# Kernel optimization log

Measured on AMD Instinct MI355X. Metric: run time of the kernel, lower is better.

## Reference

```python
import jax, jax.numpy as jnp
import numpy as np
from jax import lax

DUNITS = 1024
ATT_DIM = 512
EPROJS = 512
ACONV_CHANS = 10
ACONV_FILTS = 100  # kernel size = 2*100+1 = 201
H_LEN = 16384
N_PREV = 128
SCALING = 2.0


def setup_inputs() -> dict:
    key = jax.random.key(0)
    ks = jax.random.split(key, 10)
    inv = lambda fan_in: 1.0 / np.sqrt(fan_in)
    return {
        "dec_z": jax.random.normal(ks[0], (1, DUNITS), jnp.float32),
        "att_prev": jax.random.uniform(ks[1], (N_PREV, 1, H_LEN), jnp.float32) / H_LEN,
        "pre_compute_enc_h": jax.random.normal(ks[2], (1, H_LEN, ATT_DIM), jnp.float32),
        "enc_h": jax.random.normal(ks[3], (1, H_LEN, EPROJS), jnp.float32),
        "mask": jnp.zeros((1, H_LEN), jnp.float32),
        # parameters (torch default inits, scale by 1/sqrt(fan_in))
        "loc_conv_w": jax.random.normal(ks[4], (ACONV_CHANS, 1, 2 * ACONV_FILTS + 1), jnp.float32) * inv(2 * ACONV_FILTS + 1),
        "mlp_att_w": jax.random.normal(ks[5], (ATT_DIM, ACONV_CHANS), jnp.float32) * inv(ACONV_CHANS),
        "mlp_dec_w": jax.random.normal(ks[6], (ATT_DIM, DUNITS), jnp.float32) * inv(DUNITS),
        "gvec_w": jax.random.normal(ks[7], (1, ATT_DIM), jnp.float32) * inv(ATT_DIM),
        "gvec_b": jnp.zeros((1,), jnp.float32),
    }


def reference(dec_z, att_prev, pre_compute_enc_h, enc_h, mask,
              loc_conv_w, mlp_att_w, mlp_dec_w, gvec_w, gvec_b):
    h_length = enc_h.shape[1]
    dec_z = dec_z.reshape(1, DUNITS)

    # coverage vector: sum of all previous attention distributions -> [1, h]
    cov_vec = jnp.sum(att_prev, axis=0)

    # location conv: Conv2d(1, C, (1, 2F+1)) on [1,1,1,h] == 1D conv on [1,1,h]
    att_conv = lax.conv_general_dilated(
        cov_vec[:, None, :], loc_conv_w,
        window_strides=(1,), padding=[(ACONV_FILTS, ACONV_FILTS)],
        dimension_numbers=("NCH", "OIH", "NCH"),
    )  # [1, C, h]
    # squeeze/transpose then mlp_att (no bias): [1, h, att_dim]
    att_conv = jnp.einsum("bch,ac->bha", att_conv, mlp_att_w)

    # mlp_dec (no bias), tiled over h: [1, 1, att_dim]
    dec_z_tiled = (dec_z @ mlp_dec_w.T)[:, None, :]

    # additive attention score e: [1, h]
    t = jnp.tanh(att_conv + pre_compute_enc_h + dec_z_tiled)
    e = jnp.einsum("bha,oa->bho", t, gvec_w)[..., 0] + gvec_b
    e = e + mask

    w = jax.nn.softmax(SCALING * e, axis=1)  # [1, h]

    att_prev_new = jnp.concatenate([att_prev, w[None]], axis=0)  # [n+1, 1, h]
    c = jnp.sum(enc_h * w[:, :, None], axis=1)  # [1, eprojs]
    return (c, att_prev_new)
```

## Files before the change

### kernel.cpp

```cpp
#include <hip/hip_runtime.h>

#define H_LEN 16384
#define ATT_DIM 512
#define DUNITS 1024
#define EPROJS 512
#define NCH 10
#define KFILT 201
#define PAD 100
#define N_PREV 128
#define NB_SCORE 512
#define NB_FIN 256
#define NCOVP 16

__global__ __launch_bounds__(256) void k_prep(const float* __restrict__ att_prev,
                                              const float* __restrict__ mlp_dec_w,
                                              const float* __restrict__ dec_z,
                                              float* __restrict__ out_prev,
                                              float* __restrict__ cov16,
                                              float* __restrict__ dz,
                                              float* __restrict__ out_c) {
    int b = blockIdx.x, tid = threadIdx.x;
    if (b < 256) {
        const float4* ap4 = (const float4*)att_prev;
        float4* op4 = (float4*)out_prev;
        float4* cv4 = (float4*)cov16;
        int hb = b >> 4, q = b & 15;
        int idx0 = hb * 256 + tid;
        float4 s = {0.f, 0.f, 0.f, 0.f};
        #pragma unroll
        for (int n = q * 8; n < q * 8 + 8; ++n) {
            float4 v = ap4[n * (H_LEN / 4) + idx0];
            s.x += v.x; s.y += v.y; s.z += v.z; s.w += v.w;
            op4[n * (H_LEN / 4) + idx0] = v;
        }
        cv4[q * (H_LEN / 4) + idx0] = s;
    } else if (b < 384) {
        int lane = tid & 63;
        int a = (b - 256) * 4 + (tid >> 6);
        const float* row = mlp_dec_w + a * DUNITS;
        float s = 0.f;
        #pragma unroll
        for (int t = 0; t < DUNITS / 64; ++t) s += row[lane + 64 * t] * dec_z[lane + 64 * t];
        #pragma unroll
        for (int off = 32; off > 0; off >>= 1) s += __shfl_xor(s, off, 64);
        if (lane == 0) dz[a] = s;
    } else {
        out_c[tid] = 0.f;
        out_c[tid + 256] = 0.f;
    }
}

__global__ __launch_bounds__(256, 2) void k_score(const float* __restrict__ cov16,
                                                  const float* __restrict__ cw,
                                                  const float* __restrict__ pre,
                                                  const float* __restrict__ mask,
                                                  const float* __restrict__ dz,
                                                  const float* __restrict__ watt,
                                                  const float* __restrict__ gv,
                                                  const float* __restrict__ gb,
                                                  const float* __restrict__ enc,
                                                  float* __restrict__ vbuf,
                                                  float* __restrict__ pm,
                                                  float* __restrict__ ps,
                                                  float* __restrict__ pcb) {
    __shared__ float cov_s[32 + 2 * PAD];
    __shared__ float mask_s[32];
    __shared__ float pc[8][NCH][32];
    __shared__ float cf[NCH][32];
    __shared__ float vt[32];
    __shared__ float wt[32];

    int tid = threadIdx.x, b = blockIdx.x;
    int h0 = b * 32;
    int lane = tid & 63, wv = tid >> 6;
    int a0 = lane * 4;

    for (int i = tid; i < 32 + 2 * PAD; i += 256) {
        int g = h0 - PAD + i;
        float s = 0.f;
        if (g >= 0 && g < H_LEN) {
            #pragma unroll
            for (int q = 0; q < NCOVP; ++q) s += cov16[q * H_LEN + g];
        }
        cov_s[i] = s;
    }
    if (tid < 32) mask_s[tid] = mask[h0 + tid];

    const float4* pre4 = (const float4*)pre;
    int hbase = h0 + wv * 8;
    float4 P[16];
    #pragma unroll
    for (int j = 0; j < 8; ++j) {
        P[2 * j]     = pre4[(hbase + j) * 128 + lane];
        P[2 * j + 1] = pre4[(hbase + j) * 128 + 64 + lane];
    }

    float Wr[8][NCH], dzr[8], gvr[8];
    #pragma unroll
    for (int i = 0; i < 8; ++i) {
        int a = (i < 4) ? (a0 + i) : (a0 + 256 + (i - 4));
        dzr[i] = dz[a];
        gvr[i] = gv[a];
        #pragma unroll
        for (int c = 0; c < NCH; ++c) Wr[i][c] = watt[a * NCH + c];
    }
    float bias = gb[0];
    __syncthreads();

    {
        int h = tid & 31, q = tid >> 5;
        int k0 = (q * KFILT) / 8, k1 = ((q + 1) * KFILT) / 8;
        float acc[NCH];
        #pragma unroll
        for (int c = 0; c < NCH; ++c) acc[c] = 0.f;
        for (int k = k0; k < k1; ++k) {
            float s = cov_s[h + k];
            #pragma unroll
            for (int c = 0; c < NCH; ++c) acc[c] += s * cw[c * KFILT + k];
        }
        #pragma unroll
        for (int c = 0; c < NCH; ++c) pc[q][c][h] = acc[c];
    }
    __syncthreads();
    for (int i = tid; i < NCH * 32; i += 256) {
        int c = i >> 5, h = i & 31;
        float s = 0.f;
        #pragma unroll
        for (int q = 0; q < 8; ++q) s += pc[q][c][h];
        cf[c][h] = s;
    }
    __syncthreads();

    #pragma unroll
    for (int j = 0; j < 8; ++j) {
        int hh = wv * 8 + j;
        float ch[NCH];
        #pragma unroll
        for (int c = 0; c < NCH; ++c) ch[c] = cf[c][hh];
        float4 c0 = P[2 * j], c1 = P[2 * j + 1];
        float pv[8] = {c0.x, c0.y, c0.z, c0.w, c1.x, c1.y, c1.z, c1.w};
        float eacc = 0.f;
        #pragma unroll
        for (int i = 0; i < 8; ++i) {
            float x = pv[i] + dzr[i];
            #pragma unroll
            for (int c = 0; c < NCH; ++c) x += ch[c] * Wr[i][c];
            x = fminf(fmaxf(x, -15.f), 15.f);
            float z = __expf(2.f * x);
            float t = (z - 1.f) * __builtin_amdgcn_rcpf(z + 1.f);
            eacc += t * gvr[i];
        }
        #pragma unroll
        for (int off = 32; off > 0; off >>= 1) eacc += __shfl_xor(eacc, off, 64);
        if (lane == 0) {
            float v = 2.f * (eacc + bias + mask_s[hh]);
            vt[hh] = v;
            vbuf[h0 + hh] = v;
        }
    }
    __syncthreads();

    if (wv == 0) {
        float v = (lane < 32) ? vt[lane] : -1e30f;
        float m = v;
        #pragma unroll
        for (int off = 32; off > 0; off >>= 1) m = fmaxf(m, __shfl_xor(m, off, 64));
        float ev = (lane < 32) ? __expf(v - m) : 0.f;
        if (lane < 32) wt[lane] = ev;
        float s = ev;
        #pragma unroll
        for (int off = 32; off > 0; off >>= 1) s += __shfl_xor(s, off, 64);
        if (lane == 0) { pm[b] = m; ps[b] = s; }
    }
    __syncthreads();

    const float2* enc2 = (const float2*)enc;
    float2 acc0 = {0.f, 0.f}, acc1 = {0.f, 0.f};
    #pragma unroll
    for (int h = 0; h < 32; h += 2) {
        float w0 = wt[h], w1 = wt[h + 1];
        float2 e0 = enc2[(h0 + h) * 256 + tid];
        float2 e1 = enc2[(h0 + h + 1) * 256 + tid];
        acc0.x += w0 * e0.x; acc0.y += w0 * e0.y;
        acc1.x += w1 * e1.x; acc1.y += w1 * e1.y;
    }
    float2 acc = {acc0.x + acc1.x, acc0.y + acc1.y};
    ((float2*)pcb)[b * 256 + tid] = acc;
}

__global__ __launch_bounds__(256) void k_final(const float* __restrict__ vbuf,
                                               const float* __restrict__ pm,
                                               const float* __restrict__ ps,
                                               const float* __restrict__ pcb,
                                               float* __restrict__ out_w,
                                               float* __restrict__ out_c) {
    __shared__ float redA[4], redB[4];
    int tid = threadIdx.x, b = blockIdx.x;
    int lane = tid & 63, wv = tid >> 6;

    float m0 = pm[tid], m1 = pm[tid + 256];
    float s0 = ps[tid], s1 = ps[tid + 256];
    float m = fmaxf(m0, m1);
    #pragma unroll
    for (int off = 32; off > 0; off >>= 1) m = fmaxf(m, __shfl_xor(m, off, 64));
    if (lane == 0) redA[wv] = m;
    __syncthreads();
    float M = fmaxf(fmaxf(redA[0], redA[1]), fmaxf(redA[2], redA[3]));
    float s = s0 * __expf(m0 - M) + s1 * __expf(m1 - M);
    #pragma unroll
    for (int off = 32; off > 0; off >>= 1) s += __shfl_xor(s, off, 64);
    if (lane == 0) redB[wv] = s;
    __syncthreads();
    float S = redB[0] + redB[1] + redB[2] + redB[3];
    float rinv = 1.f / S;

    if (tid < 64) {
        int h = b * 64 + tid;
        out_w[h] = __expf(vbuf[h] - M) * rinv;
    }

    int r0 = 2 * b, r1 = 2 * b + 1;
    float sc0 = __expf(pm[r0] - M) * rinv;
    float sc1 = __expf(pm[r1] - M) * rinv;
    float v0 = pcb[r0 * EPROJS + tid] * sc0 + pcb[r1 * EPROJS + tid] * sc1;
    float v1 = pcb[r0 * EPROJS + tid + 256] * sc0 + pcb[r1 * EPROJS + tid + 256] * sc1;
    atomicAdd(&out_c[tid], v0);
    atomicAdd(&out_c[tid + 256], v1);
}

extern "C" void kernel_launch(void* const* d_in, const int* in_sizes, int n_in,
                              void* d_out, int out_size, void* d_ws, size_t ws_size,
                              hipStream_t stream) {
    const float* dec_z      = (const float*)d_in[0];
    const float* att_prev   = (const float*)d_in[1];
    const float* pre        = (const float*)d_in[2];
    const float* enc_h      = (const float*)d_in[3];
    const float* mask       = (const float*)d_in[4];
    const float* loc_conv_w = (const float*)d_in[5];
    const float* mlp_att_w  = (const float*)d_in[6];
    const float* mlp_dec_w  = (const float*)d_in[7];
    const float* gvec_w     = (const float*)d_in[8];
    const float* gvec_b     = (const float*)d_in[9];

    float* out_c    = (float*)d_out;
    float* out_prev = out_c + EPROJS;
    float* out_w    = out_prev + N_PREV * H_LEN;

    float* ws    = (float*)d_ws;
    float* cov16 = ws;
    float* dz    = cov16 + NCOVP * H_LEN;
    float* vb    = dz + ATT_DIM;
    float* pm    = vb + H_LEN;
    float* ps    = pm + NB_SCORE;
    float* pcb   = ps + NB_SCORE;

    k_prep<<<385, 256, 0, stream>>>(att_prev, mlp_dec_w, dec_z, out_prev, cov16, dz, out_c);
    k_score<<<NB_SCORE, 256, 0, stream>>>(cov16, loc_conv_w, pre, mask, dz, mlp_att_w,
                                          gvec_w, gvec_b, enc_h, vb, pm, ps, pcb);
    k_final<<<NB_FIN, 256, 0, stream>>>(vb, pm, ps, pcb, out_w, out_c);
}
```

Measured before the change: 146.3 us.

## Fuse softmax finalize into score kernel via last-block atomic counter

Removes the separate k_final launch. Each score block now bumps an atomic counter after writing its partials, and the last block to finish computes the global softmax normalisation, writes all attention weights and reduces the 512 context partials without atomics. The warp shuffle reductions for the 8 rows per wave are also batched so they interleave. This saves a kernel launch and the out_c atomics, but it serialises the final reduction of 16K weights and 256K partials onto a single block.

Measured after the change: 219.9 us. 50.4% more time.

```diff
diff --git a/kernel.cpp b/kernel.cpp
--- a/kernel.cpp
+++ b/kernel.cpp
@@ -8,8 +8,7 @@
 #define KFILT 201
 #define PAD 100
 #define N_PREV 128
-#define NB_SCORE 512
-#define NB_FIN 256
+#define NBLK 512
 #define NCOVP 16
 
 __global__ __launch_bounds__(256) void k_prep(const float* __restrict__ att_prev,
@@ -18,7 +17,7 @@
                                               float* __restrict__ out_prev,
                                               float* __restrict__ cov16,
                                               float* __restrict__ dz,
-                                              float* __restrict__ out_c) {
+                                              int* __restrict__ cnt) {
     int b = blockIdx.x, tid = threadIdx.x;
     if (b < 256) {
         const float4* ap4 = (const float4*)att_prev;
@@ -45,8 +44,7 @@
         for (int off = 32; off > 0; off >>= 1) s += __shfl_xor(s, off, 64);
         if (lane == 0) dz[a] = s;
     } else {
-        out_c[tid] = 0.f;
-        out_c[tid + 256] = 0.f;
+        if (tid == 0) *cnt = 0;
     }
 }
 
@@ -62,13 +60,20 @@
                                                   float* __restrict__ vbuf,
                                                   float* __restrict__ pm,
                                                   float* __restrict__ ps,
-                                                  float* __restrict__ pcb) {
+                                                  float* __restrict__ pcb,
+                                                  float* __restrict__ out_w,
+                                                  float* __restrict__ out_c,
+                                                  int* __restrict__ cnt) {
     __shared__ float cov_s[32 + 2 * PAD];
     __shared__ float mask_s[32];
     __shared__ float pc[8][NCH][32];
     __shared__ float cf[NCH][32];
     __shared__ float vt[32];
     __shared__ float wt[32];
+    __shared__ float scale_s[NBLK];
+    __shared__ float4 ctmp[128];
+    __shared__ float redA[4], redB[4];
+    __shared__ int isLast;
 
     int tid = threadIdx.x, b = blockIdx.x;
     int h0 = b * 32;
@@ -131,6 +136,7 @@
     }
     __syncthreads();
 
+    float ea[8];
     #pragma unroll
     for (int j = 0; j < 8; ++j) {
         int hh = wv * 8 + j;
@@ -150,10 +156,18 @@
             float t = (z - 1.f) * __builtin_amdgcn_rcpf(z + 1.f);
             eacc += t * gvr[i];
         }
-        #pragma unroll
-        for (int off = 32; off > 0; off >>= 1) eacc += __shfl_xor(eacc, off, 64);
-        if (lane == 0) {
-            float v = 2.f * (eacc + bias + mask_s[hh]);
+        ea[j] = eacc;
+    }
+    #pragma unroll
+    for (int off = 32; off > 0; off >>= 1) {
+        #pragma unroll
+        for (int j = 0; j < 8; ++j) ea[j] += __shfl_xor(ea[j], off, 64);
+    }
+    if (lane == 0) {
+        #pragma unroll
+        for (int j = 0; j < 8; ++j) {
+            int hh = wv * 8 + j;
+            float v = 2.f * (ea[j] + bias + mask_s[hh]);
             vt[hh] = v;
             vbuf[h0 + hh] = v;
         }
@@ -184,19 +198,15 @@
         acc0.x += w0 * e0.x; acc0.y += w0 * e0.y;
         acc1.x += w1 * e1.x; acc1.y += w1 * e1.y;
     }
-    float2 acc = {acc0.x + acc1.x, acc0.y + acc1.y};
-    ((float2*)pcb)[b * 256 + tid] = acc;
-}
-
-__global__ __launch_bounds__(256) void k_final(const float* __restrict__ vbuf,
-                                               const float* __restrict__ pm,
-                                               const float* __restrict__ ps,
-                                               const float* __restrict__ pcb,
-                                               float* __restrict__ out_w,
-                                               float* __restrict__ out_c) {
-    __shared__ float redA[4], redB[4];
-    int tid = threadIdx.x, b = blockIdx.x;
-    int lane = tid & 63, wv = tid >> 6;
+    float2 accv = {acc0.x + acc1.x, acc0.y + acc1.y};
+    ((float2*)pcb)[b * 256 + tid] = accv;
+
+    __threadfence();
+    __syncthreads();
+    if (tid == 0) isLast = (atomicAdd(cnt, 1) == NBLK - 1);
+    __syncthreads();
+    if (!isLast) return;
+    __threadfence();
 
     float m0 = pm[tid], m1 = pm[tid + 256];
     float s0 = ps[tid], s1 = ps[tid + 256];
@@ -206,26 +216,49 @@
     if (lane == 0) redA[wv] = m;
     __syncthreads();
     float M = fmaxf(fmaxf(redA[0], redA[1]), fmaxf(redA[2], redA[3]));
-    float s = s0 * __expf(m0 - M) + s1 * __expf(m1 - M);
+    float e0 = __expf(m0 - M), e1 = __expf(m1 - M);
+    float s = s0 * e0 + s1 * e1;
     #pragma unroll
     for (int off = 32; off > 0; off >>= 1) s += __shfl_xor(s, off, 64);
     if (lane == 0) redB[wv] = s;
     __syncthreads();
     float S = redB[0] + redB[1] + redB[2] + redB[3];
     float rinv = 1.f / S;
-
-    if (tid < 64) {
-        int h = b * 64 + tid;
-        out_w[h] = __expf(vbuf[h] - M) * rinv;
-    }
-
-    int r0 = 2 * b, r1 = 2 * b + 1;
-    float sc0 = __expf(pm[r0] - M) * rinv;
-    float sc1 = __expf(pm[r1] - M) * rinv;
-    float v0 = pcb[r0 * EPROJS + tid] * sc0 + pcb[r1 * EPROJS + tid] * sc1;
-    float v1 = pcb[r0 * EPROJS + tid + 256] * sc0 + pcb[r1 * EPROJS + tid + 256] * sc1;
-    atomicAdd(&out_c[tid], v0);
-    atomicAdd(&out_c[tid + 256], v1);
+    scale_s[tid] = e0 * rinv;
+    scale_s[tid + 256] = e1 * rinv;
+    __syncthreads();
+
+    {
+        const float4* vb4 = (const float4*)vbuf;
+        float4* ow4 = (float4*)out_w;
+        for (int i = tid; i < H_LEN / 4; i += 256) {
+            float4 v = vb4[i];
+            float4 o = { __expf(v.x - M) * rinv, __expf(v.y - M) * rinv,
+                         __expf(v.z - M) * rinv, __expf(v.w - M) * rinv };
+            ow4[i] = o;
+        }
+    }
+
+    {
+        const float4* pcb4 = (const float4*)pcb;
+        int c = tid & 127, half = tid >> 7;
+        float4 acc = {0.f, 0.f, 0.f, 0.f};
+        int r0 = half * 256;
+        #pragma unroll 4
+        for (int r = r0; r < r0 + 256; ++r) {
+            float sc = scale_s[r];
+            float4 p = pcb4[r * 128 + c];
+            acc.x += sc * p.x; acc.y += sc * p.y;
+            acc.z += sc * p.z; acc.w += sc * p.w;
+        }
+        if (half) ctmp[c] = acc;
+        __syncthreads();
+        if (!half) {
+            float4 o = ctmp[c];
+            acc.x += o.x; acc.y += o.y; acc.z += o.z; acc.w += o.w;
+            ((float4*)out_c)[c] = acc;
+        }
+    }
 }
 
 extern "C" void kernel_launch(void* const* d_in, const int* in_sizes, int n_in,
@@ -251,11 +284,12 @@
     float* dz    = cov16 + NCOVP * H_LEN;
     float* vb    = dz + ATT_DIM;
     float* pm    = vb + H_LEN;
-    float* ps    = pm + NB_SCORE;
-    float* pcb   = ps + NB_SCORE;
-
-    k_prep<<<385, 256, 0, stream>>>(att_prev, mlp_dec_w, dec_z, out_prev, cov16, dz, out_c);
-    k_score<<<NB_SCORE, 256, 0, stream>>>(cov16, loc_conv_w, pre, mask, dz, mlp_att_w,
-                                          gvec_w, gvec_b, enc_h, vb, pm, ps, pcb);
-    k_final<<<NB_FIN, 256, 0, stream>>>(vb, pm, ps, pcb, out_w, out_c);
+    float* ps    = pm + NBLK;
+    float* pcb   = ps + NBLK;
+    int*   cnt   = (int*)(pcb + NBLK * EPROJS);
+
+    k_prep<<<385, 256, 0, stream>>>(att_prev, mlp_dec_w, dec_z, out_prev, cov16, dz, cnt);
+    k_score<<<NBLK, 256, 0, stream>>>(cov16, loc_conv_w, pre, mask, dz, mlp_att_w,
+                                      gvec_w, gvec_b, enc_h, vb, pm, ps, pcb,
+                                      out_w, out_c, cnt);
 }
```

## Remap score work to column-pairs per thread with transposed-reduction across rows

Applied to the files above, without the earlier changes.

Each thread now owns two attention columns for all 32 rows instead of eight columns for eight rows. The pre-computed encoder rows are streamed in float2 chunks, and the mlp_att weights are pre-transposed in k_prep so they load as float2 per channel. Per-row dot products are combined with a butterfly transpose-reduce across lanes followed by a small shared-memory sum over waves, which replaces the eight full wave reductions per wave. This is meant to cut register pressure from the 16 float4 prefetch and the shuffle cost, at the price of holding 32 accumulators per thread and an extra workspace buffer.

Result: faster. 139.2 us (-4.8%).

```diff
diff --git a/kernel.cpp b/kernel.cpp
--- a/kernel.cpp
+++ b/kernel.cpp
@@ -8,6 +8,7 @@
 #define KFILT 201
 #define PAD 100
 #define N_PREV 128
+#define HB 32
 #define NB_SCORE 512
 #define NB_FIN 256
 #define NCOVP 16
@@ -15,9 +16,11 @@
 __global__ __launch_bounds__(256) void k_prep(const float* __restrict__ att_prev,
                                               const float* __restrict__ mlp_dec_w,
                                               const float* __restrict__ dec_z,
+                                              const float* __restrict__ watt,
                                               float* __restrict__ out_prev,
                                               float* __restrict__ cov16,
                                               float* __restrict__ dz,
+                                              float* __restrict__ wattT,
                                               float* __restrict__ out_c) {
     int b = blockIdx.x, tid = threadIdx.x;
     if (b < 256) {
@@ -47,6 +50,12 @@
     } else {
         out_c[tid] = 0.f;
         out_c[tid + 256] = 0.f;
+        int a = tid * 2;
+        #pragma unroll
+        for (int c = 0; c < NCH; ++c) {
+            wattT[c * ATT_DIM + a]     = watt[a * NCH + c];
+            wattT[c * ATT_DIM + a + 1] = watt[(a + 1) * NCH + c];
+        }
     }
 }
 
@@ -55,7 +64,7 @@
                                                   const float* __restrict__ pre,
                                                   const float* __restrict__ mask,
                                                   const float* __restrict__ dz,
-                                                  const float* __restrict__ watt,
+                                                  const float* __restrict__ wattT,
                                                   const float* __restrict__ gv,
                                                   const float* __restrict__ gb,
                                                   const float* __restrict__ enc,
@@ -63,19 +72,18 @@
                                                   float* __restrict__ pm,
                                                   float* __restrict__ ps,
                                                   float* __restrict__ pcb) {
-    __shared__ float cov_s[32 + 2 * PAD];
-    __shared__ float mask_s[32];
-    __shared__ float pc[8][NCH][32];
-    __shared__ float cf[NCH][32];
-    __shared__ float vt[32];
-    __shared__ float wt[32];
+    __shared__ float cov_s[HB + 2 * PAD];
+    __shared__ float mask_s[HB];
+    __shared__ float pc[8][NCH][HB];
+    __shared__ float cfT[HB * 12];
+    __shared__ float ew[4][HB];
+    __shared__ float wt[HB];
 
     int tid = threadIdx.x, b = blockIdx.x;
-    int h0 = b * 32;
+    int h0 = b * HB;
     int lane = tid & 63, wv = tid >> 6;
-    int a0 = lane * 4;
-
-    for (int i = tid; i < 32 + 2 * PAD; i += 256) {
+
+    for (int i = tid; i < HB + 2 * PAD; i += 256) {
         int g = h0 - PAD + i;
         float s = 0.f;
         if (g >= 0 && g < H_LEN) {
@@ -84,25 +92,16 @@
         }
         cov_s[i] = s;
     }
-    if (tid < 32) mask_s[tid] = mask[h0 + tid];
-
-    const float4* pre4 = (const float4*)pre;
-    int hbase = h0 + wv * 8;
-    float4 P[16];
-    #pragma unroll
-    for (int j = 0; j < 8; ++j) {
-        P[2 * j]     = pre4[(hbase + j) * 128 + lane];
-        P[2 * j + 1] = pre4[(hbase + j) * 128 + 64 + lane];
-    }
-
-    float Wr[8][NCH], dzr[8], gvr[8];
-    #pragma unroll
-    for (int i = 0; i < 8; ++i) {
-        int a = (i < 4) ? (a0 + i) : (a0 + 256 + (i - 4));
-        dzr[i] = dz[a];
-        gvr[i] = gv[a];
-        #pragma unroll
-        for (int c = 0; c < NCH; ++c) Wr[i][c] = watt[a * NCH + c];
+    if (tid < HB) mask_s[tid] = mask[h0 + tid];
+
+    int a = (wv << 7) + (lane << 1);
+    float2 dz2 = *(const float2*)(dz + a);
+    float2 gv2 = *(const float2*)(gv + a);
+    float W0[NCH], W1[NCH];
+    #pragma unroll
+    for (int c = 0; c < NCH; ++c) {
+        float2 w = *(const float2*)(wattT + c * ATT_DIM + a);
+        W0[c] = w.x; W1[c] = w.y;
     }
     float bias = gb[0];
     __syncthreads();
@@ -122,51 +121,87 @@
         for (int c = 0; c < NCH; ++c) pc[q][c][h] = acc[c];
     }
     __syncthreads();
-    for (int i = tid; i < NCH * 32; i += 256) {
+    for (int i = tid; i < NCH * HB; i += 256) {
         int c = i >> 5, h = i & 31;
         float s = 0.f;
         #pragma unroll
         for (int q = 0; q < 8; ++q) s += pc[q][c][h];
-        cf[c][h] = s;
-    }
-    __syncthreads();
-
-    #pragma unroll
-    for (int j = 0; j < 8; ++j) {
-        int hh = wv * 8 + j;
-        float ch[NCH];
-        #pragma unroll
-        for (int c = 0; c < NCH; ++c) ch[c] = cf[c][hh];
-        float4 c0 = P[2 * j], c1 = P[2 * j + 1];
-        float pv[8] = {c0.x, c0.y, c0.z, c0.w, c1.x, c1.y, c1.z, c1.w};
-        float eacc = 0.f;
-        #pragma unroll
-        for (int i = 0; i < 8; ++i) {
-            float x = pv[i] + dzr[i];
+        cfT[h * 12 + c] = s;
+    }
+    __syncthreads();
+
+    float ea[HB];
+    const float2* pre2 = (const float2*)pre;
+    int colf2 = (wv << 6) + lane;
+    #pragma unroll
+    for (int hc = 0; hc < HB; hc += 8) {
+        float2 Pr[8];
+        #pragma unroll
+        for (int j = 0; j < 8; ++j) Pr[j] = pre2[(h0 + hc + j) * 256 + colf2];
+        #pragma unroll
+        for (int j = 0; j < 8; ++j) {
+            int h = hc + j;
+            const float4* cp = (const float4*)&cfT[h * 12];
+            float4 c0 = cp[0], c1 = cp[1], c2 = cp[2];
+            float ch[NCH] = {c0.x, c0.y, c0.z, c0.w, c1.x, c1.y, c1.z, c1.w, c2.x, c2.y};
+            float x0 = Pr[j].x + dz2.x;
+            float x1 = Pr[j].y + dz2.y;
             #pragma unroll
-            for (int c = 0; c < NCH; ++c) x += ch[c] * Wr[i][c];
-            x = fminf(fmaxf(x, -15.f), 15.f);
-            float z = __expf(2.f * x);
-            float t = (z - 1.f) * __builtin_amdgcn_rcpf(z + 1.f);
-            eacc += t * gvr[i];
-        }
-        #pragma unroll
-        for (int off = 32; off > 0; off >>= 1) eacc += __shfl_xor(eacc, off, 64);
-        if (lane == 0) {
-            float v = 2.f * (eacc + bias + mask_s[hh]);
-            vt[hh] = v;
-            vbuf[h0 + hh] = v;
-        }
-    }
+            for (int c = 0; c < NCH; ++c) { x0 += ch[c] * W0[c]; x1 += ch[c] * W1[c]; }
+            x0 = fminf(fmaxf(x0, -15.f), 15.f);
+            x1 = fminf(fmaxf(x1, -15.f), 15.f);
+            float z0 = __expf(2.f * x0), z1 = __expf(2.f * x1);
+            float t0 = (z0 - 1.f) * __builtin_amdgcn_rcpf(z0 + 1.f);
+            float t1 = (z1 - 1.f) * __builtin_amdgcn_rcpf(z1 + 1.f);
+            ea[h] = t0 * gv2.x + t1 * gv2.y;
+        }
+    }
+
+    #pragma unroll
+    for (int k = 0; k < 16; ++k) {
+        float up = __shfl_xor(ea[k + 16], 32, 64);
+        float dn = __shfl_xor(ea[k], 32, 64);
+        ea[k] = (lane & 32) ? (ea[k + 16] + up) : (ea[k] + dn);
+    }
+    #pragma unroll
+    for (int k = 0; k < 8; ++k) {
+        float up = __shfl_xor(ea[k + 8], 16, 64);
+        float dn = __shfl_xor(ea[k], 16, 64);
+        ea[k] = (lane & 16) ? (ea[k + 8] + up) : (ea[k] + dn);
+    }
+    #pragma unroll
+    for (int k = 0; k < 4; ++k) {
+        float up = __shfl_xor(ea[k + 4], 8, 64);
+        float dn = __shfl_xor(ea[k], 8, 64);
+        ea[k] = (lane & 8) ? (ea[k + 4] + up) : (ea[k] + dn);
+    }
+    #pragma unroll
+    for (int k = 0; k < 2; ++k) {
+        float up = __shfl_xor(ea[k + 2], 4, 64);
+        float dn = __shfl_xor(ea[k], 4, 64);
+        ea[k] = (lane & 4) ? (ea[k + 2] + up) : (ea[k] + dn);
+    }
+    {
+        float up = __shfl_xor(ea[1], 2, 64);
+        float dn = __shfl_xor(ea[0], 2, 64);
+        ea[0] = (lane & 2) ? (ea[1] + up) : (ea[0] + dn);
+    }
+    ea[0] += __shfl_xor(ea[0], 1, 64);
+    if ((lane & 1) == 0) ew[wv][lane >> 1] = ea[0];
     __syncthreads();
 
     if (wv == 0) {
-        float v = (lane < 32) ? vt[lane] : -1e30f;
+        float v = -1e30f;
+        if (lane < HB) {
+            float e = ew[0][lane] + ew[1][lane] + ew[2][lane] + ew[3][lane];
+            v = 2.f * (e + bias + mask_s[lane]);
+            vbuf[h0 + lane] = v;
+        }
         float m = v;
         #pragma unroll
         for (int off = 32; off > 0; off >>= 1) m = fmaxf(m, __shfl_xor(m, off, 64));
-        float ev = (lane < 32) ? __expf(v - m) : 0.f;
-        if (lane < 32) wt[lane] = ev;
+        float ev = (lane < HB) ? __expf(v - m) : 0.f;
+        if (lane < HB) wt[lane] = ev;
         float s = ev;
         #pragma unroll
         for (int off = 32; off > 0; off >>= 1) s += __shfl_xor(s, off, 64);
@@ -177,15 +212,15 @@
     const float2* enc2 = (const float2*)enc;
     float2 acc0 = {0.f, 0.f}, acc1 = {0.f, 0.f};
     #pragma unroll
-    for (int h = 0; h < 32; h += 2) {
+    for (int h = 0; h < HB; h += 2) {
         float w0 = wt[h], w1 = wt[h + 1];
         float2 e0 = enc2[(h0 + h) * 256 + tid];
         float2 e1 = enc2[(h0 + h + 1) * 256 + tid];
         acc0.x += w0 * e0.x; acc0.y += w0 * e0.y;
         acc1.x += w1 * e1.x; acc1.y += w1 * e1.y;
     }
-    float2 acc = {acc0.x + acc1.x, acc0.y + acc1.y};
-    ((float2*)pcb)[b * 256 + tid] = acc;
+    float2 accv = {acc0.x + acc1.x, acc0.y + acc1.y};
+    ((float2*)pcb)[b * 256 + tid] = accv;
 }
 
 __global__ __launch_bounds__(256) void k_final(const float* __restrict__ vbuf,
@@ -253,9 +288,11 @@
     float* pm    = vb + H_LEN;
     float* ps    = pm + NB_SCORE;
     float* pcb   = ps + NB_SCORE;
-
-    k_prep<<<385, 256, 0, stream>>>(att_prev, mlp_dec_w, dec_z, out_prev, cov16, dz, out_c);
-    k_score<<<NB_SCORE, 256, 0, stream>>>(cov16, loc_conv_w, pre, mask, dz, mlp_att_w,
+    float* wattT = pcb + NB_SCORE * EPROJS;
+
+    k_prep<<<385, 256, 0, stream>>>(att_prev, mlp_dec_w, dec_z, mlp_att_w,
+                                    out_prev, cov16, dz, wattT, out_c);
+    k_score<<<NB_SCORE, 256, 0, stream>>>(cov16, loc_conv_w, pre, mask, dz, wattT,
                                           gvec_w, gvec_b, enc_h, vb, pm, ps, pcb);
     k_final<<<NB_FIN, 256, 0, stream>>>(vb, pm, ps, pcb, out_w, out_c);
 }
```
